# Kernel tuning notes

Measured on AMD Instinct MI355X. Metric: run time of the kernel, lower is better.

## Reference

```python
import jax, jax.numpy as jnp
import numpy as np
import math

N_ENT = 40000
N_EDGE = 640000
CHANNEL = 128
N_REL = 50
N_USERS = 10000
KG_HEADS = 2


def segment_softmax(scores, seg, num_segments):
    # numerically-stable softmax over edges grouped by segment id
    m = jax.ops.segment_max(scores, seg, num_segments=num_segments)
    e = jnp.exp(scores - m[seg])
    s = jax.ops.segment_sum(e, seg, num_segments=num_segments)
    return e / s[seg]


def setup_inputs() -> dict:
    key = jax.random.key(0)
    k1, k2, k3, k4, k5, k6 = jax.random.split(key, 6)
    entity_emb = jax.random.normal(k1, (N_ENT, CHANNEL), dtype=jnp.float32)
    user_emb = jax.random.normal(k2, (N_USERS, CHANNEL), dtype=jnp.float32)
    relation_weight = jax.random.normal(k3, (N_REL, CHANNEL), dtype=jnp.float32)
    # xavier-style scale for the square projection
    kg_W_r = jax.random.normal(k4, (CHANNEL, CHANNEL), dtype=jnp.float32) * math.sqrt(2.0 / (CHANNEL + CHANNEL))
    edge_index = jax.random.randint(k5, (2, N_EDGE), 0, N_ENT)
    edge_type = jax.random.randint(k6, (N_EDGE,), 1, N_REL + 1)  # types in [1, N_REL]
    return {
        "entity_emb": entity_emb,
        "user_emb": user_emb,
        "relation_weight": relation_weight,
        "kg_W_r": kg_W_r,
        "edge_index": edge_index,
        "edge_type": edge_type,
    }


def reference(entity_emb, user_emb, relation_weight, kg_W_r, edge_index, edge_type):
    head, tail = edge_index[0], edge_index[1]
    n_ent, channel = entity_emb.shape
    d_k = channel // KG_HEADS

    # --- relation_aware_att (g_mask=None) ---
    rel_emb = relation_weight[edge_type - 1]          # [E, C]
    head_emb = entity_emb[head]                       # [E, C]
    query = (head_emb @ kg_W_r).reshape(-1, KG_HEADS, d_k)
    key = (rel_emb @ kg_W_r).reshape(-1, KG_HEADS, d_k)
    score_r = (query * key).sum(-1) / math.sqrt(d_k)  # [E, H]
    score_r = score_r.mean(-1)                        # [E]
    rel_scores = segment_softmax(score_r, head, n_ent)

    # --- kg_inv_capture ---
    t_emb = entity_emb[tail]                          # [E, C]
    r_emb = rel_emb * rel_scores[:, None]             # [E, C]
    # bmm([h;r], [t;r]^T) == h.t + r.r per edge
    score_trip = (head_emb * t_emb).sum(-1) + (r_emb * r_emb).sum(-1)
    kg_attn_score = segment_softmax(score_trip, head, n_ent)
    return kg_attn_score
```

## Files before the change

kernel.cpp:

```cpp
#include <hip/hip_runtime.h>
#include <hip/hip_fp16.h>
#include <math.h>

#define CHANNEL 128
#define NEG_INF (-1e30f)
#define MAXD 64

typedef _Float16 half2v __attribute__((ext_vector_type(2)));
union F4H { float4 f; half2v h[4]; };

__global__ void __launch_bounds__(256) zero_kernel(int* __restrict__ p, int n) {
    int i = blockIdx.x * 256 + threadIdx.x;
    if (i < n) p[i] = 0;
}

__global__ void __launch_bounds__(256) fused_prep_kernel(
    const float* __restrict__ relw, const float* __restrict__ W,
    const int* __restrict__ eidx, const int* __restrict__ etype,
    const float* __restrict__ ent,
    __half* __restrict__ P2h, float* __restrict__ rel_norm,
    int* __restrict__ deg, int2* __restrict__ recs, __half* __restrict__ ent16,
    int E, int R, int ceblk, int NC)
{
    int b = blockIdx.x;
    if (b < R) {
        __shared__ float rw[CHANNEL];
        __shared__ float kr[CHANNEL];
        __shared__ float red[CHANNEL];
        int c = threadIdx.x;
        int j = b;
        if (c < CHANNEL) {
            float v = relw[j * CHANNEL + c];
            rw[c] = v;
            red[c] = v * v;
        }
        __syncthreads();
        for (int s = CHANNEL / 2; s > 0; s >>= 1) {
            if (c < s) red[c] += red[c + s];
            __syncthreads();
        }
        if (c == 0) rel_norm[j] = red[0];
        if (c < CHANNEL) {
            float acc = 0.f;
            for (int k = 0; k < CHANNEL; ++k) acc += rw[k] * W[k * CHANNEL + c];
            kr[c] = acc;
        }
        __syncthreads();
        if (c < CHANNEL) {
            float acc2 = 0.f;
            for (int cc = 0; cc < CHANNEL; ++cc) acc2 += W[c * CHANNEL + cc] * kr[cc];
            P2h[j * CHANNEL + c] = __float2half(acc2 * 0.0625f);
        }
    } else if (b < R + ceblk) {
        int e = (b - R) * 256 + threadIdx.x;
        if (e < E) {
            int h = eidx[e];
            int t = eidx[E + e];
            int r = etype[e] - 1;
            int k = atomicAdd(deg + h, 1);
            if (k < MAXD)
                recs[(size_t)h * MAXD + k] = make_int2(t | (r << 20), e);
        }
    } else {
        int i4 = ((b - R - ceblk) * 256 + threadIdx.x) * 4;
        if (i4 + 3 < NC) {
            float4 v = *(const float4*)(ent + i4);
            __half2 a = __floats2half2_rn(v.x, v.y);
            __half2 c2 = __floats2half2_rn(v.z, v.w);
            uint2 u = make_uint2(*(unsigned*)&a, *(unsigned*)&c2);
            *(uint2*)(ent16 + i4) = u;
        } else {
            for (int i = i4; i < NC; ++i) ent16[i] = __float2half(ent[i]);
        }
    }
}

struct Row { float4 t, r; };

__global__ void __launch_bounds__(256, 8) main_kernel(
        const __half* __restrict__ ent16, const __half* __restrict__ P2h,
        const float* __restrict__ rel_norm, const int* __restrict__ deg,
        const int2* __restrict__ recs, float* __restrict__ out, int N) {
    int wid = (int)((blockIdx.x * blockDim.x + threadIdx.x) >> 6);
    if (wid >= N) return;
    int lane = threadIdx.x & 63;
    int grp = lane >> 4;
    int sub = lane & 15;

    int deg_h = deg[wid];
    if (deg_h == 0) return;
    if (deg_h > MAXD) deg_h = MAXD;
    size_t s0 = (size_t)wid * MAXD;

    F4H hu;
    hu.f = ((const float4*)(ent16 + (size_t)wid * CHANNEL))[sub];

    int lc = lane < deg_h ? lane : deg_h - 1;
    int2 rc = recs[s0 + lc];
    int iters = (deg_h + 3) >> 2;

    auto issue = [&](int g) -> Row {
        Row s;
        int e = 4 * g + grp;
        int ec = e < deg_h ? e : deg_h - 1;
        int rcx = __shfl(rc.x, ec);
        int tail = rcx & 0xFFFFF;
        int typ = rcx >> 20;
        s.t = ((const float4*)(ent16 + (size_t)tail * CHANNEL))[sub];
        s.r = ((const float4*)(P2h + typ * CHANNEL))[sub];
        return s;
    };

    float d1c = 0.f, d2c = 0.f;
    auto compute = [&](int g, const Row& s) {
        F4H tu, ru;
        tu.f = s.t;
        ru.f = s.r;
        float d1 = 0.f, d2 = 0.f;
#pragma unroll
        for (int k = 0; k < 4; ++k) {
            d1 = __builtin_amdgcn_fdot2(hu.h[k], tu.h[k], d1, false);
            d2 = __builtin_amdgcn_fdot2(hu.h[k], ru.h[k], d2, false);
        }
#pragma unroll
        for (int m = 1; m <= 8; m <<= 1) {
            d1 += __shfl_xor(d1, m);
            d2 += __shfl_xor(d2, m);
        }
        int srcl = (lane & 3) * 16;
        float td1 = __shfl(d1, srcl);
        float td2 = __shfl(d2, srcl);
        if ((lane >> 2) == g) { d1c = td1; d2c = td2; }
    };

    Row A = issue(0);
    int g = 0;
    while (g < iters) {
        Row B = issue(g + 1);
        compute(g, A);
        ++g;
        if (g >= iters) break;
        A = issue(g + 1);
        compute(g, B);
        ++g;
    }

    bool valid = lane < deg_h;
    int typc = rc.x >> 20;
    int eidc = rc.y;
    float m1 = valid ? d2c : NEG_INF;
#pragma unroll
    for (int m = 32; m; m >>= 1) m1 = fmaxf(m1, __shfl_xor(m1, m));
    float e1 = valid ? expf(d2c - m1) : 0.f;
    float s1 = e1;
#pragma unroll
    for (int m = 32; m; m >>= 1) s1 += __shfl_xor(s1, m);
    float rs = e1 / s1;
    float stv = d1c + rs * rs * rel_norm[typc];
    float m2 = valid ? stv : NEG_INF;
#pragma unroll
    for (int m = 32; m; m >>= 1) m2 = fmaxf(m2, __shfl_xor(m2, m));
    float e2 = valid ? expf(stv - m2) : 0.f;
    float s2 = e2;
#pragma unroll
    for (int m = 32; m; m >>= 1) s2 += __shfl_xor(s2, m);
    if (valid) out[eidc] = e2 / s2;
}

extern "C" void kernel_launch(void* const* d_in, const int* in_sizes, int n_in,
                              void* d_out, int out_size, void* d_ws, size_t ws_size,
                              hipStream_t stream) {
    const float* ent   = (const float*)d_in[0];
    const float* relw  = (const float*)d_in[2];
    const float* W     = (const float*)d_in[3];
    const int*   eidx  = (const int*)d_in[4];
    const int*   etype = (const int*)d_in[5];
    float* out = (float*)d_out;

    const int E = in_sizes[5];
    const int N = in_sizes[0] / CHANNEL;
    const int R = in_sizes[2] / CHANNEL;
    const int NC = N * CHANNEL;

    char* base = (char*)d_ws;
    auto alloc = [&](size_t bytes) {
        char* p = base;
        base += (bytes + 15) & ~(size_t)15;
        return p;
    };
    int*    deg      = (int*)alloc((size_t)N * 4);
    int2*   recs     = (int2*)alloc((size_t)N * MAXD * 8);
    __half* P2h      = (__half*)alloc((size_t)R * CHANNEL * 2);
    float*  rel_norm = (float*)alloc((size_t)R * 4);
    __half* ent16    = (__half*)alloc((size_t)NC * 2);

    zero_kernel<<<(N + 255) / 256, 256, 0, stream>>>(deg, N);

    int ceblk = (E + 255) / 256;
    int cvblk = (NC / 4 + 255) / 256;
    fused_prep_kernel<<<R + ceblk + cvblk, 256, 0, stream>>>(
        relw, W, eidx, etype, ent, P2h, rel_norm, deg, recs, ent16, E, R, ceblk, NC);

    int bm = (N + 3) / 4;
    main_kernel<<<bm, 256, 0, stream>>>(ent16, P2h, rel_norm, deg, recs, out, N);
}
```

Measured before the change: 83.14 us.

## Process eight edges per wave iteration and move fp16 conversion into zero kernel

The main kernel now assigns 8 lanes per edge, each loading two float4 chunks of the tail and relation rows. A wave therefore handles 8 edges per iteration instead of 4, which halves the iteration count and the shuffle-reduction depth per edge and exposes more independent loads. Separately, the entity fp16 conversion moves from the edge-placement kernel into the deg-zeroing kernel, so the placement launch is lighter and the conversion runs earlier. The wider loads raise register use under the 8-waves launch bound, which could lower occupancy.

```diff
diff --git a/kernel.cpp b/kernel.cpp
--- a/kernel.cpp
+++ b/kernel.cpp
@@ -9,18 +9,33 @@
 typedef _Float16 half2v __attribute__((ext_vector_type(2)));
 union F4H { float4 f; half2v h[4]; };
 
-__global__ void __launch_bounds__(256) zero_kernel(int* __restrict__ p, int n) {
-    int i = blockIdx.x * 256 + threadIdx.x;
-    if (i < n) p[i] = 0;
-}
-
-__global__ void __launch_bounds__(256) fused_prep_kernel(
+__global__ void __launch_bounds__(256) zero_conv_kernel(
+    int* __restrict__ deg, const float* __restrict__ ent,
+    __half* __restrict__ ent16, int N, int NC, int zblk)
+{
+    int b = blockIdx.x;
+    if (b < zblk) {
+        int i = b * 256 + threadIdx.x;
+        if (i < N) deg[i] = 0;
+    } else {
+        int i4 = ((b - zblk) * 256 + threadIdx.x) * 4;
+        if (i4 + 3 < NC) {
+            float4 v = *(const float4*)(ent + i4);
+            __half2 a = __floats2half2_rn(v.x, v.y);
+            __half2 c2 = __floats2half2_rn(v.z, v.w);
+            uint2 u = make_uint2(*(unsigned*)&a, *(unsigned*)&c2);
+            *(uint2*)(ent16 + i4) = u;
+        } else {
+            for (int i = i4; i < NC; ++i) ent16[i] = __float2half(ent[i]);
+        }
+    }
+}
+
+__global__ void __launch_bounds__(256) prep_place_kernel(
     const float* __restrict__ relw, const float* __restrict__ W,
     const int* __restrict__ eidx, const int* __restrict__ etype,
-    const float* __restrict__ ent,
     __half* __restrict__ P2h, float* __restrict__ rel_norm,
-    int* __restrict__ deg, int2* __restrict__ recs, __half* __restrict__ ent16,
-    int E, int R, int ceblk, int NC)
+    int* __restrict__ deg, int2* __restrict__ recs, int E, int R)
 {
     int b = blockIdx.x;
     if (b < R) {
@@ -51,7 +66,7 @@
             for (int cc = 0; cc < CHANNEL; ++cc) acc2 += W[c * CHANNEL + cc] * kr[cc];
             P2h[j * CHANNEL + c] = __float2half(acc2 * 0.0625f);
         }
-    } else if (b < R + ceblk) {
+    } else {
         int e = (b - R) * 256 + threadIdx.x;
         if (e < E) {
             int h = eidx[e];
@@ -61,21 +76,10 @@
             if (k < MAXD)
                 recs[(size_t)h * MAXD + k] = make_int2(t | (r << 20), e);
         }
-    } else {
-        int i4 = ((b - R - ceblk) * 256 + threadIdx.x) * 4;
-        if (i4 + 3 < NC) {
-            float4 v = *(const float4*)(ent + i4);
-            __half2 a = __floats2half2_rn(v.x, v.y);
-            __half2 c2 = __floats2half2_rn(v.z, v.w);
-            uint2 u = make_uint2(*(unsigned*)&a, *(unsigned*)&c2);
-            *(uint2*)(ent16 + i4) = u;
-        } else {
-            for (int i = i4; i < NC; ++i) ent16[i] = __float2half(ent[i]);
-        }
     }
 }
 
-struct Row { float4 t, r; };
+struct Row { float4 t0, t1, r0, r1; };
 
 __global__ void __launch_bounds__(256, 8) main_kernel(
         const __half* __restrict__ ent16, const __half* __restrict__ P2h,
@@ -84,53 +88,72 @@
     int wid = (int)((blockIdx.x * blockDim.x + threadIdx.x) >> 6);
     if (wid >= N) return;
     int lane = threadIdx.x & 63;
-    int grp = lane >> 4;
-    int sub = lane & 15;
+    int grp = lane >> 3;
+    int sub = lane & 7;
 
     int deg_h = deg[wid];
     if (deg_h == 0) return;
     if (deg_h > MAXD) deg_h = MAXD;
     size_t s0 = (size_t)wid * MAXD;
 
-    F4H hu;
-    hu.f = ((const float4*)(ent16 + (size_t)wid * CHANNEL))[sub];
+    const float4* hrow = (const float4*)(ent16 + (size_t)wid * CHANNEL);
+    F4H hu0, hu1;
+    hu0.f = hrow[sub];
+    hu1.f = hrow[sub + 8];
 
     int lc = lane < deg_h ? lane : deg_h - 1;
     int2 rc = recs[s0 + lc];
-    int iters = (deg_h + 3) >> 2;
+    int iters = (deg_h + 7) >> 3;
 
     auto issue = [&](int g) -> Row {
         Row s;
-        int e = 4 * g + grp;
-        int ec = e < deg_h ? e : deg_h - 1;
-        int rcx = __shfl(rc.x, ec);
-        int tail = rcx & 0xFFFFF;
-        int typ = rcx >> 20;
-        s.t = ((const float4*)(ent16 + (size_t)tail * CHANNEL))[sub];
-        s.r = ((const float4*)(P2h + typ * CHANNEL))[sub];
+        if (g < iters) {
+            int e = 8 * g + grp;
+            int ec = e < deg_h ? e : deg_h - 1;
+            int rcx = __shfl(rc.x, ec);
+            int tail = rcx & 0xFFFFF;
+            int typ = rcx >> 20;
+            const float4* tp = (const float4*)(ent16 + (size_t)tail * CHANNEL);
+            const float4* rp = (const float4*)(P2h + typ * CHANNEL);
+            s.t0 = tp[sub]; s.t1 = tp[sub + 8];
+            s.r0 = rp[sub]; s.r1 = rp[sub + 8];
+        } else {
+            s.t0 = s.t1 = s.r0 = s.r1 = make_float4(0.f, 0.f, 0.f, 0.f);
+        }
         return s;
     };
 
     float d1c = 0.f, d2c = 0.f;
     auto compute = [&](int g, const Row& s) {
-        F4H tu, ru;
-        tu.f = s.t;
-        ru.f = s.r;
-        float d1 = 0.f, d2 = 0.f;
-#pragma unroll
-        for (int k = 0; k < 4; ++k) {
-            d1 = __builtin_amdgcn_fdot2(hu.h[k], tu.h[k], d1, false);
-            d2 = __builtin_amdgcn_fdot2(hu.h[k], ru.h[k], d2, false);
-        }
-#pragma unroll
-        for (int m = 1; m <= 8; m <<= 1) {
+        F4H t0, t1, r0, r1;
+        t0.f = s.t0; t1.f = s.t1; r0.f = s.r0; r1.f = s.r1;
+        float d1a = __builtin_amdgcn_fdot2(hu0.h[0], t0.h[0], 0.f, false);
+        float d1b = __builtin_amdgcn_fdot2(hu0.h[1], t0.h[1], 0.f, false);
+        float d2a = __builtin_amdgcn_fdot2(hu0.h[0], r0.h[0], 0.f, false);
+        float d2b = __builtin_amdgcn_fdot2(hu0.h[1], r0.h[1], 0.f, false);
+        d1a = __builtin_amdgcn_fdot2(hu0.h[2], t0.h[2], d1a, false);
+        d1b = __builtin_amdgcn_fdot2(hu0.h[3], t0.h[3], d1b, false);
+        d2a = __builtin_amdgcn_fdot2(hu0.h[2], r0.h[2], d2a, false);
+        d2b = __builtin_amdgcn_fdot2(hu0.h[3], r0.h[3], d2b, false);
+        d1a = __builtin_amdgcn_fdot2(hu1.h[0], t1.h[0], d1a, false);
+        d1b = __builtin_amdgcn_fdot2(hu1.h[1], t1.h[1], d1b, false);
+        d2a = __builtin_amdgcn_fdot2(hu1.h[0], r1.h[0], d2a, false);
+        d2b = __builtin_amdgcn_fdot2(hu1.h[1], r1.h[1], d2b, false);
+        d1a = __builtin_amdgcn_fdot2(hu1.h[2], t1.h[2], d1a, false);
+        d1b = __builtin_amdgcn_fdot2(hu1.h[3], t1.h[3], d1b, false);
+        d2a = __builtin_amdgcn_fdot2(hu1.h[2], r1.h[2], d2a, false);
+        d2b = __builtin_amdgcn_fdot2(hu1.h[3], r1.h[3], d2b, false);
+        float d1 = d1a + d1b;
+        float d2 = d2a + d2b;
+#pragma unroll
+        for (int m = 1; m <= 4; m <<= 1) {
             d1 += __shfl_xor(d1, m);
             d2 += __shfl_xor(d2, m);
         }
-        int srcl = (lane & 3) * 16;
+        int srcl = (lane & 7) * 8;
         float td1 = __shfl(d1, srcl);
         float td2 = __shfl(d2, srcl);
-        if ((lane >> 2) == g) { d1c = td1; d2c = td2; }
+        if ((lane >> 3) == g) { d1c = td1; d2c = td2; }
     };
 
     Row A = issue(0);
@@ -194,12 +217,13 @@
     float*  rel_norm = (float*)alloc((size_t)R * 4);
     __half* ent16    = (__half*)alloc((size_t)NC * 2);
 
-    zero_kernel<<<(N + 255) / 256, 256, 0, stream>>>(deg, N);
+    int zblk = (N + 255) / 256;
+    int cvblk = (NC / 4 + 255) / 256;
+    zero_conv_kernel<<<zblk + cvblk, 256, 0, stream>>>(deg, ent, ent16, N, NC, zblk);
 
     int ceblk = (E + 255) / 256;
-    int cvblk = (NC / 4 + 255) / 256;
-    fused_prep_kernel<<<R + ceblk + cvblk, 256, 0, stream>>>(
-        relw, W, eidx, etype, ent, P2h, rel_norm, deg, recs, ent16, E, R, ceblk, NC);
+    prep_place_kernel<<<R + ceblk, 256, 0, stream>>>(
+        relw, W, eidx, etype, P2h, rel_norm, deg, recs, E, R);
 
     int bm = (N + 3) / 4;
     main_kernel<<<bm, 256, 0, stream>>>(ent16, P2h, rel_norm, deg, recs, out, N);
```

New measurement: 101.8 us. 1.22x slower.
